# Kernel tuning notes

Hardware: AMD Instinct MI355X
Metric: run time of the kernel (lower is better)

The kernel has to match this reference:

```python
import jax, jax.numpy as jnp
import numpy as np

# ROIAlign config (torchvision semantics, aligned=False)
SPATIAL_SCALE = 0.25
POOLED = 7
SAMPLING_RATIO = 2
MODE = "max"  # from __init__ mode='max'


def setup_inputs() -> dict:
    key = jax.random.key(0)
    kf, kcx, kcy, kw, kh, kb = jax.random.split(key, 6)
    B, C, H, W = 2, 256, 200, 304
    N = 512
    IMG_H, IMG_W = H / SPATIAL_SCALE, W / SPATIAL_SCALE
    feature = jax.random.normal(kf, (B, C, H, W), dtype=jnp.float32)
    cx = jax.random.uniform(kcx, (N,)) * IMG_W
    cy = jax.random.uniform(kcy, (N,)) * IMG_H
    bw = jax.random.uniform(kw, (N,)) * 192.0 + 16.0
    bh = jax.random.uniform(kh, (N,)) * 192.0 + 16.0
    x1 = jnp.clip(cx - bw * 0.5, 0.0, IMG_W - 2.0)
    y1 = jnp.clip(cy - bh * 0.5, 0.0, IMG_H - 2.0)
    x2 = jnp.clip(cx + bw * 0.5, x1 + 1.0, IMG_W - 1.0)
    y2 = jnp.clip(cy + bh * 0.5, y1 + 1.0, IMG_H - 1.0)
    boxes = jnp.stack([x1, y1, x2, y2], axis=1).astype(jnp.float32)
    batch_idx = jax.random.randint(kb, (N,), 0, B, dtype=jnp.int32)
    return {"feature": feature, "boxes": boxes, "batch_idx": batch_idx}


def _sample_coords(start, size):
    # start,size: [N]; returns [N, POOLED*SAMPLING_RATIO] sample coordinates
    bin_sz = size / POOLED                         # [N]
    p = jnp.arange(POOLED, dtype=jnp.float32)      # bin index
    s = (jnp.arange(SAMPLING_RATIO, dtype=jnp.float32) + 0.5) / SAMPLING_RATIO
    # coord = start + (p + s) * bin_sz  -> [N, POOLED, RATIO]
    c = start[:, None, None] + (p[None, :, None] + s[None, None, :]) * bin_sz[:, None, None]
    return c.reshape(c.shape[0], POOLED * SAMPLING_RATIO)


def roi_align(feature, boxes, batch_idx):
    B, C, H, W = feature.shape
    roi = boxes * SPATIAL_SCALE                    # [N,4] in feature coords
    rs_x, rs_y, re_x, re_y = roi[:, 0], roi[:, 1], roi[:, 2], roi[:, 3]
    roi_w = jnp.maximum(re_x - rs_x, 1.0)
    roi_h = jnp.maximum(re_y - rs_y, 1.0)
    ys = _sample_coords(rs_y, roi_h)               # [N, Sy]
    xs = _sample_coords(rs_x, roi_w)               # [N, Sx]
    y = jnp.broadcast_to(ys[:, :, None], (ys.shape[0], ys.shape[1], xs.shape[1]))
    x = jnp.broadcast_to(xs[:, None, :], y.shape)  # [N, Sy, Sx]

    valid = (y > -1.0) & (y < H) & (x > -1.0) & (x < W)
    y = jnp.clip(y, 0.0, H - 1)
    x = jnp.clip(x, 0.0, W - 1)
    y0 = jnp.floor(y).astype(jnp.int32)
    x0 = jnp.floor(x).astype(jnp.int32)
    y1 = jnp.minimum(y0 + 1, H - 1)
    x1 = jnp.minimum(x0 + 1, W - 1)
    ly = y - y0.astype(y.dtype)
    lx = x - x0.astype(x.dtype)
    hy, hx = 1.0 - ly, 1.0 - lx
    b = batch_idx[:, None, None]
    # advanced indexing -> [N, Sy, Sx, C]
    val = (hy * hx)[..., None] * feature[b, :, y0, x0] \
        + (hy * lx)[..., None] * feature[b, :, y0, x1] \
        + (ly * hx)[..., None] * feature[b, :, y1, x0] \
        + (ly * lx)[..., None] * feature[b, :, y1, x1]
    val = jnp.where(valid[..., None], val, 0.0)
    N = boxes.shape[0]
    val = val.reshape(N, POOLED, SAMPLING_RATIO, POOLED, SAMPLING_RATIO, C)
    if MODE == "max":
        out = val.max(axis=(2, 4))                 # [N, PH, PW, C]
    else:
        out = val.mean(axis=(2, 4))
    return jnp.transpose(out, (0, 3, 1, 2))        # [N, C, PH, PW]


def reference(feature, boxes, batch_idx):
    return roi_align(feature, boxes, batch_idx)
```

## Files before the change

kernel.cpp:

```cpp
#include <hip/hip_runtime.h>


#define SPATIAL_SCALE 0.25f
#define POOLED 7
#define SR 2

constexpr int Bc = 2;
constexpr int Cc = 256;
constexpr int Hc = 200;
constexpr int Wc = 304;
constexpr int Nc = 512;

constexpr int CG      = 4;
constexpr int NSAMP   = POOLED * SR;
constexpr int NROW    = NSAMP * 2;
constexpr int XW      = 64;
constexpr int XPAD    = 68;
constexpr int CH_STR  = NROW * XPAD;
constexpr int CELLS   = POOLED * POOLED;
constexpr int OUTS    = CG * CELLS;
constexpr int PER_BOX = Cc * CELLS;
constexpr int PLANE   = Hc * Wc;

__global__ __launch_bounds__(256) void roi_align_max_kernel(
    const float* __restrict__ feature,
    const float* __restrict__ boxes,
    const int*   __restrict__ batch_idx,
    float*       __restrict__ out)
{
    __shared__ float lds[CG * CH_STR];

    int bid = blockIdx.x;
    int cg  = bid / Nc;
    int n   = bid - cg * Nc;
    int tid = threadIdx.x;

    float rsx = boxes[n * 4 + 0] * SPATIAL_SCALE;
    float rsy = boxes[n * 4 + 1] * SPATIAL_SCALE;
    float rex = boxes[n * 4 + 2] * SPATIAL_SCALE;
    float rey = boxes[n * 4 + 3] * SPATIAL_SCALE;
    float roi_w = fmaxf(rex - rsx, 1.0f);
    float roi_h = fmaxf(rey - rsy, 1.0f);
    float bin_w = roi_w / (float)POOLED;
    float bin_h = roi_h / (float)POOLED;
    int b = batch_idx[n];

    float x_first = __fadd_rn(rsx, __fmul_rn(0.25f, bin_w));
    float xc0 = fminf(fmaxf(x_first, 0.0f), (float)(Wc - 1));
    int xbase = ((int)floorf(xc0)) & ~3;

    const float* __restrict__ gbase =
        feature + ((size_t)b * Cc + (size_t)cg * CG) * (size_t)PLANE;

    int lane16 = tid & 15;
    int rbase  = tid >> 4;
    #pragma unroll
    for (int it = 0; it < 7; ++it) {
        int r       = it * 16 + rbase;
        int c_local = r / NROW;
        int slot    = r - c_local * NROW;
        int s       = slot >> 1;
        int which   = slot & 1;
        int p       = s >> 1;
        int sub     = s & 1;
        float py = (float)p + ((float)sub + 0.5f) * 0.5f;
        float fy = __fadd_rn(rsy, __fmul_rn(py, bin_h));
        float fyc = fminf(fmaxf(fy, 0.0f), (float)(Hc - 1));
        int y0 = (int)floorf(fyc);
        int row = which ? min(y0 + 1, Hc - 1) : y0;

        int col = xbase + lane16 * 4;
        col = min(col, Wc - 4);
        const float4 v = *(const float4*)(gbase + (size_t)c_local * PLANE
                                          + row * Wc + col);
        *(float4*)&lds[c_local * CH_STR + slot * XPAD + lane16 * 4] = v;
    }
    __syncthreads();

    if (tid < OUTS) {
        int c_local = tid / CELLS;
        int cell    = tid - c_local * CELLS;
        int ph      = cell / POOLED;
        int pw      = cell - ph * POOLED;
        const float* __restrict__ L = &lds[c_local * CH_STR];

        float m = -INFINITY;
        #pragma unroll
        for (int sy = 0; sy < SR; ++sy) {
            int sY = ph * SR + sy;
            float py = (float)ph + ((float)sy + 0.5f) * 0.5f;
            float fy = __fadd_rn(rsy, __fmul_rn(py, bin_h));
            bool vy = (fy > -1.0f) && (fy < (float)Hc);
            float fyc = fminf(fmaxf(fy, 0.0f), (float)(Hc - 1));
            int y0 = (int)floorf(fyc);
            float ly = fyc - (float)y0;
            float hy = 1.0f - ly;
            const float* __restrict__ r0 = L + (2 * sY) * XPAD;
            const float* __restrict__ r1 = L + (2 * sY + 1) * XPAD;

            #pragma unroll
            for (int sx = 0; sx < SR; ++sx) {
                float px = (float)pw + ((float)sx + 0.5f) * 0.5f;
                float fx = __fadd_rn(rsx, __fmul_rn(px, bin_w));
                bool vx = (fx > -1.0f) && (fx < (float)Wc);
                float fxc = fminf(fmaxf(fx, 0.0f), (float)(Wc - 1));
                int x0 = (int)floorf(fxc);
                float lx = fxc - (float)x0;
                float hx = 1.0f - lx;
                int c0 = x0 - xbase;
                int x1 = min(x0 + 1, Wc - 1);
                int c1 = x1 - xbase;

                float v00 = r0[c0], v01 = r0[c1];
                float v10 = r1[c0], v11 = r1[c1];
                float bil = hy * hx * v00 + hy * lx * v01 +
                            ly * hx * v10 + ly * lx * v11;
                float v = (vy && vx) ? bil : 0.0f;
                m = fmaxf(m, v);
            }
        }
        out[(size_t)n * PER_BOX + cg * OUTS + tid] = m;
    }
}

extern "C" void kernel_launch(void* const* d_in, const int* in_sizes, int n_in,
                              void* d_out, int out_size, void* d_ws, size_t ws_size,
                              hipStream_t stream) {
    const float* feature   = (const float*)d_in[0];
    const float* boxes     = (const float*)d_in[1];
    const int*   batch_idx = (const int*)d_in[2];
    float*       out       = (float*)d_out;

    int grid = (Cc / CG) * Nc;
    roi_align_max_kernel<<<grid, 256, 0, stream>>>(feature, boxes, batch_idx, out);
}
```

Baseline: 227.8 us.

## Precompute per-box sampling tables in setup kernel and remap blocks across XCDs

Adds a small setup kernel that computes, for each box, the row offsets, column indices and validity-masked bilinear weights, and writes them to workspace. The main kernel then reads these tables instead of redoing the float coordinate math per thread. The main kernel also remaps block IDs so that consecutive channel groups land on the same XCD for L2 locality. It changes the per-wave channel assignment (one channel per wave), uses a padded LDS stride of 66 with float2 stores, and computes bilinear values with FMAs. The cost is an extra kernel launch and workspace reads, and the FMA form may round slightly differently from before.

Result: slower. 241.1 us (+5.9%).

```diff
diff --git a/kernel.cpp b/kernel.cpp
--- a/kernel.cpp
+++ b/kernel.cpp
@@ -1,7 +1,6 @@
 #include <hip/hip_runtime.h>
 
 
-#define SPATIAL_SCALE 0.25f
 #define POOLED 7
 #define SR 2
 
@@ -10,116 +9,164 @@
 constexpr int Hc = 200;
 constexpr int Wc = 304;
 constexpr int Nc = 512;
+constexpr int PLANE   = Hc * Wc;
+constexpr int CELLS   = POOLED * POOLED;
+constexpr int PER_BOX = Cc * CELLS;
+constexpr int CG      = 4;
+constexpr int NROW    = 28;
+constexpr int XPAD    = 66;
+constexpr int ROW_B   = XPAD * 4;
+constexpr int CH_B    = NROW * ROW_B;
+constexpr int WSTRIDE = 128;
 
-constexpr int CG      = 4;
-constexpr int NSAMP   = POOLED * SR;
-constexpr int NROW    = NSAMP * 2;
-constexpr int XW      = 64;
-constexpr int XPAD    = 68;
-constexpr int CH_STR  = NROW * XPAD;
-constexpr int CELLS   = POOLED * POOLED;
-constexpr int OUTS    = CG * CELLS;
-constexpr int PER_BOX = Cc * CELLS;
-constexpr int PLANE   = Hc * Wc;
+__global__ __launch_bounds__(256) void roi_setup_kernel(
+    const float* __restrict__ boxes,
+    const int*   __restrict__ batch_idx,
+    int*         __restrict__ ws)
+{
+    int n = blockIdx.x * 4 + (threadIdx.x >> 6);
+    int t = threadIdx.x & 63;
+
+    float rsx = boxes[n * 4 + 0] * 0.25f;
+    float rsy = boxes[n * 4 + 1] * 0.25f;
+    float rex = boxes[n * 4 + 2] * 0.25f;
+    float rey = boxes[n * 4 + 3] * 0.25f;
+    float bin_w = fmaxf(rex - rsx, 1.0f) / (float)POOLED;
+    float bin_h = fmaxf(rey - rsy, 1.0f) / (float)POOLED;
+
+    float xf  = __fadd_rn(rsx, __fmul_rn(0.25f, bin_w));
+    float xc0 = fminf(fmaxf(xf, 0.0f), (float)(Wc - 1));
+    int xbase = ((int)floorf(xc0)) & ~3;
+
+    int* W = ws + n * WSTRIDE;
+
+    if (t < 14) {
+        float px = (float)(t >> 1) + ((float)(t & 1) + 0.5f) * 0.5f;
+        float fx = __fadd_rn(rsx, __fmul_rn(px, bin_w));
+        bool vx  = (fx > -1.0f) && (fx < (float)Wc);
+        float fxc = fminf(fmaxf(fx, 0.0f), (float)(Wc - 1));
+        int   x0  = (int)floorf(fxc);
+        float lx  = fxc - (float)x0;
+        float hx  = 1.0f - lx;
+        int4 e;
+        e.x = x0 - xbase;
+        e.y = min(x0 + 1, Wc - 1) - xbase;
+        e.z = __float_as_int(vx ? hx : 0.0f);
+        e.w = __float_as_int(vx ? lx : 0.0f);
+        *(int4*)(W + 32 + 4 * t) = e;
+    } else if (t >= 16 && t < 30) {
+        int s = t - 16;
+        float py = (float)(s >> 1) + ((float)(s & 1) + 0.5f) * 0.5f;
+        float fy = __fadd_rn(rsy, __fmul_rn(py, bin_h));
+        bool vy  = (fy > -1.0f) && (fy < (float)Hc);
+        float fyc = fminf(fmaxf(fy, 0.0f), (float)(Hc - 1));
+        int   y0  = (int)floorf(fyc);
+        float ly  = fyc - (float)y0;
+        float hy  = 1.0f - ly;
+        int2 e;
+        e.x = __float_as_int(vy ? hy : 0.0f);
+        e.y = __float_as_int(vy ? ly : 0.0f);
+        *(int2*)(W + 96 + 2 * s) = e;
+    } else if (t >= 32 && t < 60) {
+        int slot = t - 32;
+        int s    = slot >> 1;
+        float py = (float)(s >> 1) + ((float)(s & 1) + 0.5f) * 0.5f;
+        float fy = __fadd_rn(rsy, __fmul_rn(py, bin_h));
+        float fyc = fminf(fmaxf(fy, 0.0f), (float)(Hc - 1));
+        int   y0  = (int)floorf(fyc);
+        int   row = (slot & 1) ? min(y0 + 1, Hc - 1) : y0;
+        W[slot] = row * (Wc * 4);
+    } else if (t == 60) {
+        W[28] = xbase;
+        W[29] = batch_idx[n];
+    }
+}
 
 __global__ __launch_bounds__(256) void roi_align_max_kernel(
     const float* __restrict__ feature,
-    const float* __restrict__ boxes,
-    const int*   __restrict__ batch_idx,
+    const int*   __restrict__ ws,
     float*       __restrict__ out)
 {
-    __shared__ float lds[CG * CH_STR];
+    __shared__ float lds[CG * NROW * XPAD];
 
     int bid = blockIdx.x;
-    int cg  = bid / Nc;
-    int n   = bid - cg * Nc;
-    int tid = threadIdx.x;
+    int xcd = bid & 7;
+    int i   = bid >> 3;
+    int cg  = (xcd << 3) | (i >> 9);
+    int n   = i & 511;
 
-    float rsx = boxes[n * 4 + 0] * SPATIAL_SCALE;
-    float rsy = boxes[n * 4 + 1] * SPATIAL_SCALE;
-    float rex = boxes[n * 4 + 2] * SPATIAL_SCALE;
-    float rey = boxes[n * 4 + 3] * SPATIAL_SCALE;
-    float roi_w = fmaxf(rex - rsx, 1.0f);
-    float roi_h = fmaxf(rey - rsy, 1.0f);
-    float bin_w = roi_w / (float)POOLED;
-    float bin_h = roi_h / (float)POOLED;
-    int b = batch_idx[n];
+    const int* __restrict__ W = ws + n * WSTRIDE;
+    int tid  = threadIdx.x;
+    int cl   = tid >> 6;
+    int lane = tid & 63;
+    int sb   = lane >> 4;
+    int l16  = lane & 15;
 
-    float x_first = __fadd_rn(rsx, __fmul_rn(0.25f, bin_w));
-    float xc0 = fminf(fmaxf(x_first, 0.0f), (float)(Wc - 1));
-    int xbase = ((int)floorf(xc0)) & ~3;
+    int xbase = W[28];
+    int b     = W[29];
+    const char* gbase = (const char*)(feature
+        + ((size_t)b * Cc + (size_t)(cg * CG + cl)) * (size_t)PLANE);
+    int colb = min(xbase * 4 + l16 * 16, (Wc - 4) * 4);
+    int ldsb = cl * CH_B + sb * ROW_B + l16 * 16;
 
-    const float* __restrict__ gbase =
-        feature + ((size_t)b * Cc + (size_t)cg * CG) * (size_t)PLANE;
-
-    int lane16 = tid & 15;
-    int rbase  = tid >> 4;
     #pragma unroll
     for (int it = 0; it < 7; ++it) {
-        int r       = it * 16 + rbase;
-        int c_local = r / NROW;
-        int slot    = r - c_local * NROW;
-        int s       = slot >> 1;
-        int which   = slot & 1;
-        int p       = s >> 1;
-        int sub     = s & 1;
-        float py = (float)p + ((float)sub + 0.5f) * 0.5f;
-        float fy = __fadd_rn(rsy, __fmul_rn(py, bin_h));
-        float fyc = fminf(fmaxf(fy, 0.0f), (float)(Hc - 1));
-        int y0 = (int)floorf(fyc);
-        int row = which ? min(y0 + 1, Hc - 1) : y0;
-
-        int col = xbase + lane16 * 4;
-        col = min(col, Wc - 4);
-        const float4 v = *(const float4*)(gbase + (size_t)c_local * PLANE
-                                          + row * Wc + col);
-        *(float4*)&lds[c_local * CH_STR + slot * XPAD + lane16 * 4] = v;
+        int slot = it * 4 + sb;
+        int rowb = W[slot];
+        const float4 v = *(const float4*)(gbase + rowb + colb);
+        char* p = (char*)lds + ldsb + it * (4 * ROW_B);
+        *(float2*)(p)     = make_float2(v.x, v.y);
+        *(float2*)(p + 8) = make_float2(v.z, v.w);
     }
     __syncthreads();
 
-    if (tid < OUTS) {
-        int c_local = tid / CELLS;
-        int cell    = tid - c_local * CELLS;
-        int ph      = cell / POOLED;
-        int pw      = cell - ph * POOLED;
-        const float* __restrict__ L = &lds[c_local * CH_STR];
+    if (lane < CELLS) {
+        int ph = lane / 7;
+        int pw = lane - ph * 7;
 
+        const int4 ex0 = *(const int4*)(W + 32 + 4 * (2 * pw + 0));
+        const int4 ex1 = *(const int4*)(W + 32 + 4 * (2 * pw + 1));
+        const int2 ey0 = *(const int2*)(W + 96 + 2 * (2 * ph + 0));
+        const int2 ey1 = *(const int2*)(W + 96 + 2 * (2 * ph + 1));
+
+        const float* L = (const float*)((const char*)lds + cl * CH_B
+                                        + ph * (4 * ROW_B));
         float m = -INFINITY;
-        #pragma unroll
-        for (int sy = 0; sy < SR; ++sy) {
-            int sY = ph * SR + sy;
-            float py = (float)ph + ((float)sy + 0.5f) * 0.5f;
-            float fy = __fadd_rn(rsy, __fmul_rn(py, bin_h));
-            bool vy = (fy > -1.0f) && (fy < (float)Hc);
-            float fyc = fminf(fmaxf(fy, 0.0f), (float)(Hc - 1));
-            int y0 = (int)floorf(fyc);
-            float ly = fyc - (float)y0;
-            float hy = 1.0f - ly;
-            const float* __restrict__ r0 = L + (2 * sY) * XPAD;
-            const float* __restrict__ r1 = L + (2 * sY + 1) * XPAD;
-
-            #pragma unroll
-            for (int sx = 0; sx < SR; ++sx) {
-                float px = (float)pw + ((float)sx + 0.5f) * 0.5f;
-                float fx = __fadd_rn(rsx, __fmul_rn(px, bin_w));
-                bool vx = (fx > -1.0f) && (fx < (float)Wc);
-                float fxc = fminf(fmaxf(fx, 0.0f), (float)(Wc - 1));
-                int x0 = (int)floorf(fxc);
-                float lx = fxc - (float)x0;
-                float hx = 1.0f - lx;
-                int c0 = x0 - xbase;
-                int x1 = min(x0 + 1, Wc - 1);
-                int c1 = x1 - xbase;
-
-                float v00 = r0[c0], v01 = r0[c1];
-                float v10 = r1[c0], v11 = r1[c1];
-                float bil = hy * hx * v00 + hy * lx * v01 +
-                            ly * hx * v10 + ly * lx * v11;
-                float v = (vy && vx) ? bil : 0.0f;
-                m = fmaxf(m, v);
+        {
+            float wy0 = __int_as_float(ey0.x), wy1 = __int_as_float(ey0.y);
+            const float* r0 = L;
+            const float* r1 = L + XPAD;
+            {
+                float wx0 = __int_as_float(ex0.z), wx1 = __int_as_float(ex0.w);
+                float t0 = fmaf(wx1, r0[ex0.y], wx0 * r0[ex0.x]);
+                float t1 = fmaf(wx1, r1[ex0.y], wx0 * r1[ex0.x]);
+                m = fmaxf(m, fmaf(wy1, t1, wy0 * t0));
+            }
+            {
+                float wx0 = __int_as_float(ex1.z), wx1 = __int_as_float(ex1.w);
+                float t0 = fmaf(wx1, r0[ex1.y], wx0 * r0[ex1.x]);
+                float t1 = fmaf(wx1, r1[ex1.y], wx0 * r1[ex1.x]);
+                m = fmaxf(m, fmaf(wy1, t1, wy0 * t0));
             }
         }
-        out[(size_t)n * PER_BOX + cg * OUTS + tid] = m;
+        {
+            float wy0 = __int_as_float(ey1.x), wy1 = __int_as_float(ey1.y);
+            const float* r0 = L + 2 * XPAD;
+            const float* r1 = L + 3 * XPAD;
+            {
+                float wx0 = __int_as_float(ex0.z), wx1 = __int_as_float(ex0.w);
+                float t0 = fmaf(wx1, r0[ex0.y], wx0 * r0[ex0.x]);
+                float t1 = fmaf(wx1, r1[ex0.y], wx0 * r1[ex0.x]);
+                m = fmaxf(m, fmaf(wy1, t1, wy0 * t0));
+            }
+            {
+                float wx0 = __int_as_float(ex1.z), wx1 = __int_as_float(ex1.w);
+                float t0 = fmaf(wx1, r0[ex1.y], wx0 * r0[ex1.x]);
+                float t1 = fmaf(wx1, r1[ex1.y], wx0 * r1[ex1.x]);
+                m = fmaxf(m, fmaf(wy1, t1, wy0 * t0));
+            }
+        }
+        out[(size_t)n * PER_BOX + (size_t)(cg * CG + cl) * CELLS + lane] = m;
     }
 }
 
@@ -130,7 +177,10 @@
     const float* boxes     = (const float*)d_in[1];
     const int*   batch_idx = (const int*)d_in[2];
     float*       out       = (float*)d_out;
+    int*         ws        = (int*)d_ws;
+
+    roi_setup_kernel<<<Nc / 4, 256, 0, stream>>>(boxes, batch_idx, ws);
 
     int grid = (Cc / CG) * Nc;
-    roi_align_max_kernel<<<grid, 256, 0, stream>>>(feature, boxes, batch_idx, out);
+    roi_align_max_kernel<<<grid, 256, 0, stream>>>(feature, ws, out);
 }
```
